# Optimization experiments

Measured on AMD Instinct MI355X. Metric: run time of the kernel, lower is better.

Reference implementation:

```python
import jax, jax.numpy as jnp
import numpy as np

L, N, E, D_MODEL, H = 3, 50000, 600000, 128, 8
D = D_MODEL // H          # per-head dim = 16
DFF = 4 * D_MODEL         # feedforward hidden = 512


def prelu(x, a):
    return jnp.where(x >= 0, x, a * x)


def layernorm(x, scale, bias, eps=1e-5):
    m = x.mean(-1, keepdims=True)
    v = x.var(-1, keepdims=True)
    return (x - m) * jax.lax.rsqrt(v + eps) * scale + bias


def setup_inputs() -> dict:
    key = jax.random.key(0)
    ks = jax.random.split(key, 16)
    s = 1.0 / np.sqrt(D_MODEL)
    return {
        "in_feats": jax.random.normal(ks[0], (N, D_MODEL), jnp.float32),
        "src": jax.random.randint(ks[1], (E,), 0, N, jnp.int32),
        "dst": jax.random.randint(ks[2], (E,), 0, N, jnp.int32),
        # per-layer stacked parameters
        "W": jax.random.normal(ks[3], (L, D_MODEL, D_MODEL), jnp.float32) * s,
        "attn_l": jax.random.normal(ks[4], (L, H, D), jnp.float32) * s,
        "attn_r": jax.random.normal(ks[5], (L, H, D), jnp.float32) * s,
        "conv_bias": jnp.zeros((L, H, D), jnp.float32),
        "a_conv": jnp.full((L,), 0.25, jnp.float32),   # PReLU slope after conv
        "ln_scale": jnp.ones((L, D_MODEL), jnp.float32),
        "ln_bias": jnp.zeros((L, D_MODEL), jnp.float32),
        "W1": jax.random.normal(ks[6], (L, D_MODEL, DFF), jnp.float32) * s,
        "b1": jnp.zeros((L, DFF), jnp.float32),
        "W2": jax.random.normal(ks[7], (L, DFF, D_MODEL), jnp.float32) / np.sqrt(DFF),
        "b2": jnp.zeros((L, D_MODEL), jnp.float32),
        "a_ff": jnp.full((L,), 0.25, jnp.float32),     # PReLU slope in FF
    }


def _gat_conv(x, src, dst, W, attn_l, attn_r, conv_bias, a_conv):
    # DGL GATConv: project, per-edge additive attention, edge-softmax over dst, scatter.
    z = (x @ W).reshape(N, H, D)                    # [N,H,D]
    el = (z * attn_l).sum(-1)                       # [N,H]
    er = (z * attn_r).sum(-1)                       # [N,H]
    e = jax.nn.leaky_relu(el[src] + er[dst], 0.2)   # [E,H]
    emax = jax.ops.segment_max(e, dst, num_segments=N)
    emax = jnp.where(jnp.isfinite(emax), emax, 0.0)  # zero in-degree guard
    ex = jnp.exp(e - emax[dst])                     # [E,H]
    denom = jax.ops.segment_sum(ex, dst, num_segments=N)  # [N,H]
    msg = ex[:, :, None] * z[src]                   # [E,H,D]
    agg = jax.ops.segment_sum(msg, dst, num_segments=N)   # [N,H,D]
    out = agg / jnp.maximum(denom, 1e-9)[:, :, None]
    out = prelu(out + conv_bias, a_conv)            # bias + PReLU activation
    return out.reshape(N, H * D)


def reference(in_feats, src, dst, W, attn_l, attn_r, conv_bias, a_conv,
              ln_scale, ln_bias, W1, b1, W2, b2, a_ff):
    outputs = []
    x = in_feats
    for l in range(L):
        h = _gat_conv(x, src, dst, W[l], attn_l[l], attn_r[l], conv_bias[l], a_conv[l])
        h = layernorm(h, ln_scale[l], ln_bias[l])   # layer['norm']
        # FeedForward, norm_first=True, sharing the same LayerNorm params
        hn = layernorm(h, ln_scale[l], ln_bias[l])
        ff = prelu(hn @ W1[l] + b1[l], a_ff[l]) @ W2[l] + b2[l]
        x = h + ff
        outputs.append(x)
    return jnp.stack(outputs)                       # [L, N, d]
```

## Files before the change

kernel.cpp:

```cpp
#include <hip/hip_runtime.h>

#define DM 128
#define NH 8
#define DFF 512

typedef __attribute__((ext_vector_type(8))) short bf16x8;
typedef __attribute__((ext_vector_type(4))) float f32x4;

#define WAITVM(N) do { asm volatile("s_waitcnt vmcnt(" #N ")" ::: "memory"); \
                       __builtin_amdgcn_sched_barrier(0); } while (0)

__device__ __forceinline__ short f2bf(float f) {
    union { float f; unsigned u; } v; v.f = f;
    unsigned r = v.u + 0x7fffu + ((v.u >> 16) & 1u);
    return (short)(r >> 16);
}
__device__ __forceinline__ float bf2f(unsigned short b) {
    union { unsigned u; float f; } v; v.u = ((unsigned)b) << 16; return v.f;
}

template<int ROWS, int NT>
__device__ __forceinline__ void stage_tile(
    const short* __restrict__ g, int row0, int maxrow, int rstride, int kbase,
    short* s, int tid)
{
    const int lane = tid & 63;
#pragma unroll
    for (int rr = 0; rr < ROWS * 16 / NT; ++rr) {
        int idx = rr * NT + tid;
        int row = idx >> 4, kc = idx & 15;
        int rg = row0 + row;
        rg = (rg < maxrow) ? rg : (maxrow - 1);
        const short* src = g + (size_t)rg * rstride + kbase
                         + ((kc ^ (row & 15)) << 3);
        short* dst = s + (size_t)(idx - lane) * 8;
        __builtin_amdgcn_global_load_lds(
            (const __attribute__((address_space(1))) void*)src,
            (__attribute__((address_space(3))) void*)dst, 16, 0, 0);
    }
}

__device__ __forceinline__ bf16x8 frag_ld(const short* s, int row, int ks, int g)
{
    return *(const bf16x8*)(s + row * 128 + ((((ks << 2) + g) ^ (row & 15)) << 3));
}

template<bool PRELU, int NOUT>
__global__ __launch_bounds__(512, 4) void gemm_k128_stream(
    const short* __restrict__ A, const short* __restrict__ Bt,
    const float* __restrict__ bias, const float* __restrict__ affp,
    int M, short* __restrict__ outbf)
{
    __shared__ __align__(16) short sW[128 * 128];
    __shared__ __align__(16) short sA[3][64 * 128];

    const int tid = threadIdx.x;
    const int wave = tid >> 6, lane = tid & 63;
    const int wm = wave >> 1, wn = wave & 1;
    const int bn = blockIdx.x * 128;
    const int fr = lane & 15, g = lane >> 4;
    const int lr4 = g << 2, lc = fr;
    const int nT = (M + 63) >> 6;
    const int GY = gridDim.y;
    const int t0 = blockIdx.y;
    const int nLoc = (t0 < nT) ? ((nT - 1 - t0) / GY + 1) : 0;

    float bb[4]; float aff = 0.0f;
    if constexpr (PRELU) {
        aff = *affp;
#pragma unroll
        for (int cg = 0; cg < 4; ++cg)
            bb[cg] = bias[bn + wn * 64 + cg * 16 + lc];
    }

    stage_tile<128, 512>(Bt + (size_t)bn * 128, 0, 128, 128, 0, sW, tid);
    if (nLoc > 0) stage_tile<64, 512>(A, t0 * 64, M, 128, 0, sA[0], tid);
    if (nLoc > 1) stage_tile<64, 512>(A, (t0 + GY) * 64, M, 128, 0, sA[1], tid);

    for (int i = 0; i < nLoc; ++i) {
        const int t = t0 + i * GY;
        if (i >= 1 && i + 1 < nLoc)
            stage_tile<64, 512>(A, (t + GY) * 64, M, 128, 0, sA[(i + 1) % 3], tid);

        if (i == 0) { if (nLoc > 1) WAITVM(2); else WAITVM(0); }
        else WAITVM(16);
        __builtin_amdgcn_s_barrier();

        const short* sAb = sA[i % 3];
        f32x4 acc[4];
#pragma unroll
        for (int cg = 0; cg < 4; ++cg) acc[cg] = (f32x4)0.0f;

#pragma unroll
        for (int ks = 0; ks < 4; ++ks) {
            bf16x8 af = frag_ld(sAb, wm * 16 + fr, ks, g);
#pragma unroll
            for (int cg = 0; cg < 4; ++cg) {
                bf16x8 bf = frag_ld(sW, wn * 64 + cg * 16 + fr, ks, g);
                acc[cg] = __builtin_amdgcn_mfma_f32_16x16x32_bf16(
                    af, bf, acc[cg], 0, 0, 0);
            }
        }

#pragma unroll
        for (int cg = 0; cg < 4; ++cg) {
            int colL = wn * 64 + cg * 16 + lc;
#pragma unroll
            for (int r = 0; r < 4; ++r) {
                int row = t * 64 + wm * 16 + lr4 + r;
                if (row < M) {
                    float v = acc[cg][r];
                    if constexpr (PRELU) {
                        v += bb[cg];
                        v = (v >= 0.0f) ? v : aff * v;
                    }
                    outbf[(size_t)row * NOUT + bn + colL] = f2bf(v);
                }
            }
        }
    }
}

__global__ __launch_bounds__(512) void ffn2_pipe(
    const short* __restrict__ H1, const short* __restrict__ W2t,
    const short* __restrict__ h_bf, const float* __restrict__ b2,
    int M, float* __restrict__ xo, short* __restrict__ xbf)
{
    __shared__ __align__(16) short sA[3][64 * 128];
    __shared__ __align__(16) short sB[3][128 * 128];

    const int tid = threadIdx.x;
    const int wave = tid >> 6, lane = tid & 63;
    const int wm = wave >> 1, wn = wave & 1;
    const int bm = blockIdx.x * 64;
    const int fr = lane & 15, g = lane >> 4;
    const int lr4 = g << 2, lc = fr;

    f32x4 acc[4];
#pragma unroll
    for (int cg = 0; cg < 4; ++cg) acc[cg] = (f32x4)0.0f;

    stage_tile<64, 512>(H1, bm, M, DFF, 0, sA[0], tid);
    stage_tile<128, 512>(W2t, 0, 128, DFF, 0, sB[0], tid);

#pragma unroll
    for (int c = 0; c < 4; ++c) {
        if (c < 3) {
            stage_tile<64, 512>(H1, bm, M, DFF, (c + 1) * 128, sA[(c + 1) % 3], tid);
            stage_tile<128, 512>(W2t, 0, 128, DFF, (c + 1) * 128, sB[(c + 1) % 3], tid);
        }
        if (c < 3) WAITVM(6); else WAITVM(0);
        __builtin_amdgcn_s_barrier();

        const short* a = sA[c % 3];
        const short* b = sB[c % 3];
#pragma unroll
        for (int ks = 0; ks < 4; ++ks) {
            bf16x8 af = frag_ld(a, wm * 16 + fr, ks, g);
#pragma unroll
            for (int cg = 0; cg < 4; ++cg) {
                bf16x8 bf = frag_ld(b, wn * 64 + cg * 16 + fr, ks, g);
                acc[cg] = __builtin_amdgcn_mfma_f32_16x16x32_bf16(
                    af, bf, acc[cg], 0, 0, 0);
            }
        }
    }

#pragma unroll
    for (int cg = 0; cg < 4; ++cg) {
        int colL = wn * 64 + cg * 16 + lc;
        float bbv = b2[colL];
#pragma unroll
        for (int r = 0; r < 4; ++r) {
            int row = bm + wm * 16 + lr4 + r;
            int rc = (row < M) ? row : (M - 1);
            float v = acc[cg][r] + bbv
                    + bf2f((unsigned short)h_bf[(size_t)rc * DM + colL]);
            if (row < M) {
                xo[(size_t)row * DM + colL]  = v;
                xbf[(size_t)row * DM + colL] = f2bf(v);
            }
        }
    }
}

__global__ void wt_conv_kernel(const float* __restrict__ in, short* __restrict__ out,
                               int R, int C, int nL)
{
    int idx = blockIdx.x * blockDim.x + threadIdx.x;
    if (idx >= nL * R * C) return;
    int l = idx / (R * C);
    int rem = idx - l * (R * C);
    int r = rem / C, c = rem - r * C;
    out[(size_t)l * R * C + (size_t)c * R + r] = f2bf(in[idx]);
}

__global__ void f2bf_kernel(const float* __restrict__ in, short* __restrict__ out, int n)
{
    int idx = blockIdx.x * blockDim.x + threadIdx.x;
    if (idx < n) out[idx] = f2bf(in[idx]);
}

__global__ void el_er_kernel(const short* __restrict__ z,
                             const float* __restrict__ al,
                             const float* __restrict__ ar,
                             float* __restrict__ el, float* __restrict__ er, int N)
{
    int idx = blockIdx.x * blockDim.x + threadIdx.x;
    if (idx >= N * NH) return;
    int n = idx >> 3, h = idx & 7;
    const unsigned* zp = (const unsigned*)(z + (size_t)n * DM + h * 16);
    const float* alp = al + h * 16;
    const float* arp = ar + h * 16;
    float sl = 0.0f, sr = 0.0f;
#pragma unroll
    for (int d2 = 0; d2 < 8; ++d2) {
        unsigned u = zp[d2];
        float z0 = bf2f((unsigned short)(u & 0xffff));
        float z1 = bf2f((unsigned short)(u >> 16));
        sl = fmaf(z0, alp[2 * d2], sl);     sl = fmaf(z1, alp[2 * d2 + 1], sl);
        sr = fmaf(z0, arp[2 * d2], sr);     sr = fmaf(z1, arp[2 * d2 + 1], sr);
    }
    el[idx] = sl;
    er[idx] = sr;
}

__global__ void hist_kernel(const int* __restrict__ dst, int* __restrict__ deg, int E)
{
    int e = blockIdx.x * blockDim.x + threadIdx.x;
    if (e < E) atomicAdd(&deg[dst[e]], 1);
}

__global__ void scan1_kernel(const int* __restrict__ deg, int* __restrict__ incl,
                             int* __restrict__ bsum, int N)
{
    __shared__ int sm[256];
    int i = blockIdx.x * 256 + threadIdx.x;
    int v = (i < N) ? deg[i] : 0;
    sm[threadIdx.x] = v;
    __syncthreads();
    for (int off = 1; off < 256; off <<= 1) {
        int t = (threadIdx.x >= off) ? sm[threadIdx.x - off] : 0;
        __syncthreads();
        sm[threadIdx.x] += t;
        __syncthreads();
    }
    if (i < N) incl[i] = sm[threadIdx.x];
    if (threadIdx.x == 255) bsum[blockIdx.x] = sm[255];
}

__global__ void scan2_kernel(int* __restrict__ bsum, int nb)
{
    __shared__ int sm[256];
    int v = (threadIdx.x < nb) ? bsum[threadIdx.x] : 0;
    sm[threadIdx.x] = v;
    __syncthreads();
    for (int off = 1; off < 256; off <<= 1) {
        int t = (threadIdx.x >= off) ? sm[threadIdx.x - off] : 0;
        __syncthreads();
        sm[threadIdx.x] += t;
        __syncthreads();
    }
    if (threadIdx.x < nb) bsum[threadIdx.x] = sm[threadIdx.x];
}

__global__ void scan3_kernel(const int* __restrict__ incl, const int* __restrict__ bsum,
                             int* __restrict__ row_ptr, int N)
{
    int i = blockIdx.x * 256 + threadIdx.x;
    if (i < N) {
        int off = (blockIdx.x > 0) ? bsum[blockIdx.x - 1] : 0;
        row_ptr[i + 1] = incl[i] + off;
    }
    if (i == 0) row_ptr[0] = 0;
}

__global__ void scatter_kernel(const int* __restrict__ src, const int* __restrict__ dst,
                               const int* __restrict__ row_ptr, int* __restrict__ cursor,
                               int* __restrict__ csr_src, int E)
{
    int e = blockIdx.x * blockDim.x + threadIdx.x;
    if (e >= E) return;
    int t = dst[e];
    int pos = atomicAdd(&cursor[t], 1);
    csr_src[row_ptr[t] + pos] = src[e];
}

__global__ __launch_bounds__(256) void gat_agg_ln_kernel(
    const int* __restrict__ row_ptr, const int* __restrict__ csr_src,
    const short* __restrict__ z, const float* __restrict__ el,
    const float* __restrict__ er, const float* __restrict__ cb,
    const float* __restrict__ a_conv,
    const float* __restrict__ scale, const float* __restrict__ bias,
    short* __restrict__ h_out, short* __restrict__ hn_out, int N)
{
    int wave = threadIdx.x >> 6, lane = threadIdx.x & 63;
    int t = blockIdx.x * 4 + wave;
    if (t >= N) return;
    int h = lane >> 3;
    int c0 = 2 * lane, c1 = c0 + 1;
    float er_t = er[t * NH + h];
    int e0 = row_ptr[t], e1 = row_ptr[t + 1];
    float acc0 = 0.0f, acc1 = 0.0f, den = 0.0f;
    const unsigned* zw = (const unsigned*)z;

    int e = e0;
    for (; e + 8 <= e1; e += 8) {
        int s[8];
#pragma unroll
        for (int k = 0; k < 8; ++k) s[k] = csr_src[e + k];
        float x[8]; unsigned u[8];
#pragma unroll
        for (int k = 0; k < 8; ++k) x[k] = el[s[k] * NH + h];
#pragma unroll
        for (int k = 0; k < 8; ++k) u[k] = zw[(size_t)s[k] * 64 + lane];
#pragma unroll
        for (int k = 0; k < 8; ++k) {
            float v = x[k] + er_t;
            v = (v >= 0.0f) ? v : 0.2f * v;
            float w = __expf(v);
            den += w;
            acc0 = fmaf(w, bf2f((unsigned short)(u[k] & 0xffff)), acc0);
            acc1 = fmaf(w, bf2f((unsigned short)(u[k] >> 16)),   acc1);
        }
    }
    for (; e + 4 <= e1; e += 4) {
        int s[4];
#pragma unroll
        for (int k = 0; k < 4; ++k) s[k] = csr_src[e + k];
        float x[4]; unsigned u[4];
#pragma unroll
        for (int k = 0; k < 4; ++k) x[k] = el[s[k] * NH + h];
#pragma unroll
        for (int k = 0; k < 4; ++k) u[k] = zw[(size_t)s[k] * 64 + lane];
#pragma unroll
        for (int k = 0; k < 4; ++k) {
            float v = x[k] + er_t;
            v = (v >= 0.0f) ? v : 0.2f * v;
            float w = __expf(v);
            den += w;
            acc0 = fmaf(w, bf2f((unsigned short)(u[k] & 0xffff)), acc0);
            acc1 = fmaf(w, bf2f((unsigned short)(u[k] >> 16)),   acc1);
        }
    }
    for (; e < e1; ++e) {
        int s = csr_src[e];
        float v = el[s * NH + h] + er_t;
        v = (v >= 0.0f) ? v : 0.2f * v;
        float w = __expf(v);
        den += w;
        unsigned u = zw[(size_t)s * 64 + lane];
        acc0 = fmaf(w, bf2f((unsigned short)(u & 0xffff)), acc0);
        acc1 = fmaf(w, bf2f((unsigned short)(u >> 16)), acc1);
    }

    float a = *a_conv;
    float inv = 1.0f / fmaxf(den, 1e-9f);
    float o0 = acc0 * inv + cb[c0];
    float o1 = acc1 * inv + cb[c1];
    o0 = (o0 >= 0.0f) ? o0 : a * o0;
    o1 = (o1 >= 0.0f) ? o1 : a * o1;

    float sc0 = scale[c0], sc1 = scale[c1];
    float bi0 = bias[c0], bi1 = bias[c1];

    float s1 = o0 + o1, ss = o0 * o0 + o1 * o1;
#pragma unroll
    for (int off = 32; off > 0; off >>= 1) {
        s1 += __shfl_xor(s1, off, 64);
        ss += __shfl_xor(ss, off, 64);
    }
    float mean = s1 * (1.0f / 128.0f);
    float var = ss * (1.0f / 128.0f) - mean * mean;
    float rstd = rsqrtf(var + 1e-5f);
    float h0 = (o0 - mean) * rstd * sc0 + bi0;
    float h1 = (o1 - mean) * rstd * sc1 + bi1;
    unsigned hlo = (unsigned short)f2bf(h0);
    unsigned hhi = (unsigned short)f2bf(h1);
    ((unsigned*)h_out)[(size_t)t * 64 + lane] = hlo | (hhi << 16);

    s1 = h0 + h1; ss = h0 * h0 + h1 * h1;
#pragma unroll
    for (int off = 32; off > 0; off >>= 1) {
        s1 += __shfl_xor(s1, off, 64);
        ss += __shfl_xor(ss, off, 64);
    }
    mean = s1 * (1.0f / 128.0f);
    var = ss * (1.0f / 128.0f) - mean * mean;
    rstd = rsqrtf(var + 1e-5f);
    unsigned lo = (unsigned short)f2bf((h0 - mean) * rstd * sc0 + bi0);
    unsigned hi = (unsigned short)f2bf((h1 - mean) * rstd * sc1 + bi1);
    ((unsigned*)hn_out)[(size_t)t * 64 + lane] = lo | (hi << 16);
}

extern "C" void kernel_launch(void* const* d_in, const int* in_sizes, int n_in,
                              void* d_out, int out_size, void* d_ws, size_t ws_size,
                              hipStream_t stream)
{
    const float* in_feats = (const float*)d_in[0];
    const int*   src      = (const int*)d_in[1];
    const int*   dst      = (const int*)d_in[2];
    const float* W        = (const float*)d_in[3];
    const float* attn_l   = (const float*)d_in[4];
    const float* attn_r   = (const float*)d_in[5];
    const float* convb    = (const float*)d_in[6];
    const float* a_conv   = (const float*)d_in[7];
    const float* ln_scale = (const float*)d_in[8];
    const float* ln_bias  = (const float*)d_in[9];
    const float* W1       = (const float*)d_in[10];
    const float* b1       = (const float*)d_in[11];
    const float* W2       = (const float*)d_in[12];
    const float* b2       = (const float*)d_in[13];
    const float* a_ff     = (const float*)d_in[14];
    float* out = (float*)d_out;

    const int N = in_sizes[0] / DM;
    const int E = in_sizes[1];
    const int L = in_sizes[7];

    char* wsb = (char*)d_ws;
    size_t off = 0;
    auto alloc = [&](size_t bytes) { char* p = wsb + off; off += (bytes + 255) & ~(size_t)255; return p; };

    short* z_bf  = (short*)alloc((size_t)N * DM * sizeof(short));
    short* h_bf  = (short*)alloc((size_t)N * DM * sizeof(short));
    short* hn_bf = (short*)alloc((size_t)N * DM * sizeof(short));
    short* x_bf  = (short*)alloc((size_t)N * DM * sizeof(short));
    short* H1    = (short*)alloc((size_t)N * DFF * sizeof(short));
    float* el    = (float*)alloc((size_t)N * NH * sizeof(float));
    float* er    = (float*)alloc((size_t)N * NH * sizeof(float));
    short* Wt    = (short*)alloc((size_t)L * DM * DM * sizeof(short));
    short* W1t   = (short*)alloc((size_t)L * DFF * DM * sizeof(short));
    short* W2t   = (short*)alloc((size_t)L * DM * DFF * sizeof(short));
    int* deg     = (int*)alloc((size_t)N * sizeof(int));
    int* incl    = (int*)alloc((size_t)N * sizeof(int));
    int* bsum    = (int*)alloc(256 * sizeof(int));
    int* row_ptr = (int*)alloc((size_t)(N + 1) * sizeof(int));
    int* cursor  = (int*)alloc((size_t)N * sizeof(int));
    int* csr_src = (int*)alloc((size_t)E * sizeof(int));

    const int gM64  = (N + 63) / 64;
    const int nbScan = (N + 255) / 256;

    hipMemsetAsync(deg, 0, (size_t)N * sizeof(int), stream);
    hipMemsetAsync(cursor, 0, (size_t)N * sizeof(int), stream);
    hist_kernel<<<(E + 255) / 256, 256, 0, stream>>>(dst, deg, E);
    scan1_kernel<<<nbScan, 256, 0, stream>>>(deg, incl, bsum, N);
    scan2_kernel<<<1, 256, 0, stream>>>(bsum, nbScan);
    scan3_kernel<<<nbScan, 256, 0, stream>>>(incl, bsum, row_ptr, N);
    scatter_kernel<<<(E + 255) / 256, 256, 0, stream>>>(src, dst, row_ptr, cursor, csr_src, E);

    wt_conv_kernel<<<(L * DM * DM + 255) / 256, 256, 0, stream>>>(W, Wt, DM, DM, L);
    wt_conv_kernel<<<(L * DM * DFF + 255) / 256, 256, 0, stream>>>(W1, W1t, DM, DFF, L);
    wt_conv_kernel<<<(L * DFF * DM + 255) / 256, 256, 0, stream>>>(W2, W2t, DFF, DM, L);
    f2bf_kernel<<<(N * DM + 255) / 256, 256, 0, stream>>>(in_feats, x_bf, N * DM);

    gemm_k128_stream<false, DM><<<dim3(1, 512), 512, 0, stream>>>(
        x_bf, Wt, nullptr, nullptr, N, z_bf);

    for (int l = 0; l < L; ++l) {
        float* xo = out + (size_t)l * N * DM;

        el_er_kernel<<<(N * NH + 255) / 256, 256, 0, stream>>>(
            z_bf, attn_l + (size_t)l * NH * 16, attn_r + (size_t)l * NH * 16, el, er, N);

        gat_agg_ln_kernel<<<(N + 3) / 4, 256, 0, stream>>>(
            row_ptr, csr_src, z_bf, el, er, convb + (size_t)l * DM, a_conv + l,
            ln_scale + (size_t)l * DM, ln_bias + (size_t)l * DM, h_bf, hn_bf, N);

        gemm_k128_stream<true, DFF><<<dim3(4, 128), 512, 0, stream>>>(
            hn_bf, W1t + (size_t)l * DFF * DM, b1 + (size_t)l * DFF, a_ff + l, N, H1);

        ffn2_pipe<<<gM64, 512, 0, stream>>>(
            H1, W2t + (size_t)l * DM * DFF, h_bf, b2 + (size_t)l * DM, N, xo, x_bf);

        if (l + 1 < L)
            gemm_k128_stream<false, DM><<<dim3(1, 512), 512, 0, stream>>>(
                x_bf, Wt + (size_t)(l + 1) * DM * DM, nullptr, nullptr, N, z_bf);
    }
}
```

Before: 506.3 us.

## Fuse next-layer projection into FFN2, retile GEMM waves, merge conversion kernels

```diff
diff --git a/kernel.cpp b/kernel.cpp
--- a/kernel.cpp
+++ b/kernel.cpp
@@ -8,6 +8,8 @@
 typedef __attribute__((ext_vector_type(4))) float f32x4;
 
 #define WAITVM(N) do { asm volatile("s_waitcnt vmcnt(" #N ")" ::: "memory"); \
+                       __builtin_amdgcn_sched_barrier(0); } while (0)
+#define WAITLGKM0 do { asm volatile("s_waitcnt lgkmcnt(0)" ::: "memory"); \
                        __builtin_amdgcn_sched_barrier(0); } while (0)
 
 __device__ __forceinline__ short f2bf(float f) {
@@ -56,21 +58,21 @@
 
     const int tid = threadIdx.x;
     const int wave = tid >> 6, lane = tid & 63;
-    const int wm = wave >> 1, wn = wave & 1;
+    const int wm = wave >> 2, wn = wave & 3;
     const int bn = blockIdx.x * 128;
     const int fr = lane & 15, g = lane >> 4;
-    const int lr4 = g << 2, lc = fr;
+    const int lr4 = g << 2;
     const int nT = (M + 63) >> 6;
     const int GY = gridDim.y;
     const int t0 = blockIdx.y;
     const int nLoc = (t0 < nT) ? ((nT - 1 - t0) / GY + 1) : 0;
 
-    float bb[4]; float aff = 0.0f;
+    float bb[2]; float aff = 0.0f;
     if constexpr (PRELU) {
         aff = *affp;
 #pragma unroll
-        for (int cg = 0; cg < 4; ++cg)
-            bb[cg] = bias[bn + wn * 64 + cg * 16 + lc];
+        for (int cg = 0; cg < 2; ++cg)
+            bb[cg] = bias[bn + wn * 32 + cg * 16 + fr];
     }
 
     stage_tile<128, 512>(Bt + (size_t)bn * 128, 0, 128, 128, 0, sW, tid);
@@ -82,123 +84,208 @@
         if (i >= 1 && i + 1 < nLoc)
             stage_tile<64, 512>(A, (t + GY) * 64, M, 128, 0, sA[(i + 1) % 3], tid);
 
-        if (i == 0) { if (nLoc > 1) WAITVM(2); else WAITVM(0); }
-        else WAITVM(16);
+        if (i == 0) { if (nLoc > 1) { WAITVM(2); } else { WAITVM(0); } }
+        else if (i + 1 < nLoc) { WAITVM(18); }
+        else { WAITVM(16); }
         __builtin_amdgcn_s_barrier();
 
         const short* sAb = sA[i % 3];
-        f32x4 acc[4];
-#pragma unroll
-        for (int cg = 0; cg < 4; ++cg) acc[cg] = (f32x4)0.0f;
+        f32x4 acc[2][2];
+#pragma unroll
+        for (int ii = 0; ii < 2; ++ii)
+#pragma unroll
+            for (int cg = 0; cg < 2; ++cg) acc[ii][cg] = (f32x4)0.0f;
 
 #pragma unroll
         for (int ks = 0; ks < 4; ++ks) {
-            bf16x8 af = frag_ld(sAb, wm * 16 + fr, ks, g);
-#pragma unroll
-            for (int cg = 0; cg < 4; ++cg) {
-                bf16x8 bf = frag_ld(sW, wn * 64 + cg * 16 + fr, ks, g);
-                acc[cg] = __builtin_amdgcn_mfma_f32_16x16x32_bf16(
-                    af, bf, acc[cg], 0, 0, 0);
-            }
-        }
-
-#pragma unroll
-        for (int cg = 0; cg < 4; ++cg) {
-            int colL = wn * 64 + cg * 16 + lc;
-#pragma unroll
-            for (int r = 0; r < 4; ++r) {
-                int row = t * 64 + wm * 16 + lr4 + r;
-                if (row < M) {
-                    float v = acc[cg][r];
-                    if constexpr (PRELU) {
-                        v += bb[cg];
-                        v = (v >= 0.0f) ? v : aff * v;
+            bf16x8 af[2], bf[2];
+#pragma unroll
+            for (int ii = 0; ii < 2; ++ii)
+                af[ii] = frag_ld(sAb, wm * 32 + ii * 16 + fr, ks, g);
+#pragma unroll
+            for (int cg = 0; cg < 2; ++cg)
+                bf[cg] = frag_ld(sW, wn * 32 + cg * 16 + fr, ks, g);
+#pragma unroll
+            for (int ii = 0; ii < 2; ++ii)
+#pragma unroll
+                for (int cg = 0; cg < 2; ++cg)
+                    acc[ii][cg] = __builtin_amdgcn_mfma_f32_16x16x32_bf16(
+                        af[ii], bf[cg], acc[ii][cg], 0, 0, 0);
+        }
+
+#pragma unroll
+        for (int ii = 0; ii < 2; ++ii)
+#pragma unroll
+            for (int cg = 0; cg < 2; ++cg) {
+                int colL = wn * 32 + cg * 16 + fr;
+#pragma unroll
+                for (int r = 0; r < 4; ++r) {
+                    int row = t * 64 + wm * 32 + ii * 16 + lr4 + r;
+                    if (row < M) {
+                        float v = acc[ii][cg][r];
+                        if constexpr (PRELU) {
+                            v += bb[cg];
+                            v = (v >= 0.0f) ? v : aff * v;
+                        }
+                        outbf[(size_t)row * NOUT + bn + colL] = f2bf(v);
                     }
-                    outbf[(size_t)row * NOUT + bn + colL] = f2bf(v);
                 }
             }
-        }
-    }
-}
-
-__global__ __launch_bounds__(512) void ffn2_pipe(
+    }
+}
+
+__global__ __launch_bounds__(512, 2) void ffn2z(
     const short* __restrict__ H1, const short* __restrict__ W2t,
     const short* __restrict__ h_bf, const float* __restrict__ b2,
-    int M, float* __restrict__ xo, short* __restrict__ xbf)
-{
-    __shared__ __align__(16) short sA[3][64 * 128];
-    __shared__ __align__(16) short sB[3][128 * 128];
+    const short* __restrict__ Wnt, int has_next, int M,
+    float* __restrict__ xo, short* __restrict__ z_next)
+{
+    __shared__ __align__(16) short sWn[128 * 128];
+    __shared__ __align__(16) short sA[2][64 * 128];
+    __shared__ __align__(16) short sB[2][128 * 128];
 
     const int tid = threadIdx.x;
     const int wave = tid >> 6, lane = tid & 63;
-    const int wm = wave >> 1, wn = wave & 1;
+    const int wm = wave >> 2, wn = wave & 3;
     const int bm = blockIdx.x * 64;
     const int fr = lane & 15, g = lane >> 4;
-    const int lr4 = g << 2, lc = fr;
-
-    f32x4 acc[4];
-#pragma unroll
-    for (int cg = 0; cg < 4; ++cg) acc[cg] = (f32x4)0.0f;
-
+    const int lr4 = g << 2;
+
+    f32x4 acc[2][2];
+#pragma unroll
+    for (int ii = 0; ii < 2; ++ii)
+#pragma unroll
+        for (int cg = 0; cg < 2; ++cg) acc[ii][cg] = (f32x4)0.0f;
+
+    stage_tile<128, 512>(Wnt, 0, 128, DM, 0, sWn, tid);
     stage_tile<64, 512>(H1, bm, M, DFF, 0, sA[0], tid);
     stage_tile<128, 512>(W2t, 0, 128, DFF, 0, sB[0], tid);
 
 #pragma unroll
     for (int c = 0; c < 4; ++c) {
+        __builtin_amdgcn_s_barrier();
         if (c < 3) {
-            stage_tile<64, 512>(H1, bm, M, DFF, (c + 1) * 128, sA[(c + 1) % 3], tid);
-            stage_tile<128, 512>(W2t, 0, 128, DFF, (c + 1) * 128, sB[(c + 1) % 3], tid);
-        }
-        if (c < 3) WAITVM(6); else WAITVM(0);
+            stage_tile<64, 512>(H1, bm, M, DFF, (c + 1) * 128, sA[(c + 1) & 1], tid);
+            stage_tile<128, 512>(W2t, 0, 128, DFF, (c + 1) * 128, sB[(c + 1) & 1], tid);
+            WAITVM(6);
+        } else {
+            WAITVM(0);
+        }
         __builtin_amdgcn_s_barrier();
 
-        const short* a = sA[c % 3];
-        const short* b = sB[c % 3];
+        const short* a = sA[c & 1];
+        const short* b = sB[c & 1];
 #pragma unroll
         for (int ks = 0; ks < 4; ++ks) {
-            bf16x8 af = frag_ld(a, wm * 16 + fr, ks, g);
-#pragma unroll
-            for (int cg = 0; cg < 4; ++cg) {
-                bf16x8 bf = frag_ld(b, wn * 64 + cg * 16 + fr, ks, g);
-                acc[cg] = __builtin_amdgcn_mfma_f32_16x16x32_bf16(
-                    af, bf, acc[cg], 0, 0, 0);
+            bf16x8 af[2], bf[2];
+#pragma unroll
+            for (int ii = 0; ii < 2; ++ii)
+                af[ii] = frag_ld(a, wm * 32 + ii * 16 + fr, ks, g);
+#pragma unroll
+            for (int cg = 0; cg < 2; ++cg)
+                bf[cg] = frag_ld(b, wn * 32 + cg * 16 + fr, ks, g);
+#pragma unroll
+            for (int ii = 0; ii < 2; ++ii)
+#pragma unroll
+                for (int cg = 0; cg < 2; ++cg)
+                    acc[ii][cg] = __builtin_amdgcn_mfma_f32_16x16x32_bf16(
+                        af[ii], bf[cg], acc[ii][cg], 0, 0, 0);
+        }
+    }
+
+    short* sX = sA[0];
+#pragma unroll
+    for (int ii = 0; ii < 2; ++ii)
+#pragma unroll
+        for (int cg = 0; cg < 2; ++cg) {
+            int colL = wn * 32 + cg * 16 + fr;
+            float bbv = b2[colL];
+#pragma unroll
+            for (int r = 0; r < 4; ++r) {
+                int rowL = wm * 32 + ii * 16 + lr4 + r;
+                int row = bm + rowL;
+                int rc = (row < M) ? row : (M - 1);
+                float v = acc[ii][cg][r] + bbv
+                        + bf2f((unsigned short)h_bf[(size_t)rc * DM + colL]);
+                if (row < M) xo[(size_t)row * DM + colL] = v;
+                if (has_next) {
+                    int kc = colL >> 3;
+                    sX[rowL * 128 + ((kc ^ (rowL & 15)) << 3) + (colL & 7)]
+                        = f2bf(v);
+                }
             }
         }
-    }
-
-#pragma unroll
-    for (int cg = 0; cg < 4; ++cg) {
-        int colL = wn * 64 + cg * 16 + lc;
-        float bbv = b2[colL];
-#pragma unroll
-        for (int r = 0; r < 4; ++r) {
-            int row = bm + wm * 16 + lr4 + r;
-            int rc = (row < M) ? row : (M - 1);
-            float v = acc[cg][r] + bbv
-                    + bf2f((unsigned short)h_bf[(size_t)rc * DM + colL]);
-            if (row < M) {
-                xo[(size_t)row * DM + colL]  = v;
-                xbf[(size_t)row * DM + colL] = f2bf(v);
+    if (!has_next) return;
+
+    WAITLGKM0;
+    __builtin_amdgcn_s_barrier();
+
+    f32x4 acc3[2][2];
+#pragma unroll
+    for (int ii = 0; ii < 2; ++ii)
+#pragma unroll
+        for (int cg = 0; cg < 2; ++cg) acc3[ii][cg] = (f32x4)0.0f;
+
+#pragma unroll
+    for (int ks = 0; ks < 4; ++ks) {
+        bf16x8 af[2], bf[2];
+#pragma unroll
+        for (int ii = 0; ii < 2; ++ii)
+            af[ii] = frag_ld(sX, wm * 32 + ii * 16 + fr, ks, g);
+#pragma unroll
+        for (int cg = 0; cg < 2; ++cg)
+            bf[cg] = frag_ld(sWn, wn * 32 + cg * 16 + fr, ks, g);
+#pragma unroll
+        for (int ii = 0; ii < 2; ++ii)
+#pragma unroll
+            for (int cg = 0; cg < 2; ++cg)
+                acc3[ii][cg] = __builtin_amdgcn_mfma_f32_16x16x32_bf16(
+                    af[ii], bf[cg], acc3[ii][cg], 0, 0, 0);
+    }
+#pragma unroll
+    for (int ii = 0; ii < 2; ++ii)
+#pragma unroll
+        for (int cg = 0; cg < 2; ++cg) {
+            int colL = wn * 32 + cg * 16 + fr;
+#pragma unroll
+            for (int r = 0; r < 4; ++r) {
+                int row = bm + wm * 32 + ii * 16 + lr4 + r;
+                if (row < M)
+                    z_next[(size_t)row * DM + colL] = f2bf(acc3[ii][cg][r]);
             }
         }
-    }
-}
-
-__global__ void wt_conv_kernel(const float* __restrict__ in, short* __restrict__ out,
-                               int R, int C, int nL)
+}
+
+__global__ void conv_all_kernel(
+    const float* __restrict__ W, const float* __restrict__ W1,
+    const float* __restrict__ W2, const float* __restrict__ xin,
+    short* __restrict__ Wt, short* __restrict__ W1t, short* __restrict__ W2t,
+    short* __restrict__ xbf, int nFeat, int nL)
 {
     int idx = blockIdx.x * blockDim.x + threadIdx.x;
-    if (idx >= nL * R * C) return;
-    int l = idx / (R * C);
-    int rem = idx - l * (R * C);
-    int r = rem / C, c = rem - r * C;
-    out[(size_t)l * R * C + (size_t)c * R + r] = f2bf(in[idx]);
-}
-
-__global__ void f2bf_kernel(const float* __restrict__ in, short* __restrict__ out, int n)
-{
-    int idx = blockIdx.x * blockDim.x + threadIdx.x;
-    if (idx < n) out[idx] = f2bf(in[idx]);
+    const int n0 = nL * DM * DM, n1 = nL * DM * DFF, n2 = nL * DFF * DM;
+    if (idx < n0) {
+        int l = idx / (DM * DM), rem = idx & (DM * DM - 1);
+        int r = rem >> 7, c = rem & 127;
+        Wt[(size_t)l * DM * DM + c * DM + r] = f2bf(W[idx]);
+        return;
+    }
+    idx -= n0;
+    if (idx < n1) {
+        int l = idx / (DM * DFF), rem = idx & (DM * DFF - 1);
+        int r = rem >> 9, c = rem & 511;
+        W1t[(size_t)l * DM * DFF + (size_t)c * DM + r] = f2bf(W1[idx]);
+        return;
+    }
+    idx -= n1;
+    if (idx < n2) {
+        int l = idx / (DFF * DM), rem = idx & (DFF * DM - 1);
+        int r = rem >> 7, c = rem & 127;
+        W2t[(size_t)l * DFF * DM + (size_t)c * DFF + r] = f2bf(W2[idx]);
+        return;
+    }
+    idx -= n2;
+    if (idx < nFeat) xbf[idx] = f2bf(xin[idx]);
 }
 
 __global__ void el_er_kernel(const short* __restrict__ z,
@@ -305,15 +392,23 @@
     const unsigned* zw = (const unsigned*)z;
 
     int e = e0;
-    for (; e + 8 <= e1; e += 8) {
-        int s[8];
+    int s[8];
+    bool have = (e + 8 <= e1);
+    if (have) {
 #pragma unroll
         for (int k = 0; k < 8; ++k) s[k] = csr_src[e + k];
+    }
+    while (have) {
         float x[8]; unsigned u[8];
 #pragma unroll
         for (int k = 0; k < 8; ++k) x[k] = el[s[k] * NH + h];
 #pragma unroll
         for (int k = 0; k < 8; ++k) u[k] = zw[(size_t)s[k] * 64 + lane];
+        int en = e + 8;
+        bool hv2 = (en + 8 <= e1);
+        int sn[8];
+#pragma unroll
+        for (int k = 0; k < 8; ++k) sn[k] = hv2 ? csr_src[en + k] : 0;
 #pragma unroll
         for (int k = 0; k < 8; ++k) {
             float v = x[k] + er_t;
@@ -323,16 +418,19 @@
             acc0 = fmaf(w, bf2f((unsigned short)(u[k] & 0xffff)), acc0);
             acc1 = fmaf(w, bf2f((unsigned short)(u[k] >> 16)),   acc1);
         }
+#pragma unroll
+        for (int k = 0; k < 8; ++k) s[k] = sn[k];
+        e = en; have = hv2;
     }
     for (; e + 4 <= e1; e += 4) {
-        int s[4];
-#pragma unroll
-        for (int k = 0; k < 4; ++k) s[k] = csr_src[e + k];
+        int s4[4];
+#pragma unroll
+        for (int k = 0; k < 4; ++k) s4[k] = csr_src[e + k];
         float x[4]; unsigned u[4];
 #pragma unroll
-        for (int k = 0; k < 4; ++k) x[k] = el[s[k] * NH + h];
-#pragma unroll
-        for (int k = 0; k < 4; ++k) u[k] = zw[(size_t)s[k] * 64 + lane];
+        for (int k = 0; k < 4; ++k) x[k] = el[s4[k] * NH + h];
+#pragma unroll
+        for (int k = 0; k < 4; ++k) u[k] = zw[(size_t)s4[k] * 64 + lane];
 #pragma unroll
         for (int k = 0; k < 4; ++k) {
             float v = x[k] + er_t;
@@ -344,12 +442,12 @@
         }
     }
     for (; e < e1; ++e) {
-        int s = csr_src[e];
-        float v = el[s * NH + h] + er_t;
+        int sv = csr_src[e];
+        float v = el[sv * NH + h] + er_t;
         v = (v >= 0.0f) ? v : 0.2f * v;
         float w = __expf(v);
         den += w;
-        unsigned u = zw[(size_t)s * 64 + lane];
+        unsigned u = zw[(size_t)sv * 64 + lane];
         acc0 = fmaf(w, bf2f((unsigned short)(u & 0xffff)), acc0);
         acc1 = fmaf(w, bf2f((unsigned short)(u >> 16)), acc1);
     }
@@ -450,19 +548,21 @@
     scan3_kernel<<<nbScan, 256, 0, stream>>>(incl, bsum, row_ptr, N);
     scatter_kernel<<<(E + 255) / 256, 256, 0, stream>>>(src, dst, row_ptr, cursor, csr_src, E);
 
-    wt_conv_kernel<<<(L * DM * DM + 255) / 256, 256, 0, stream>>>(W, Wt, DM, DM, L);
-    wt_conv_kernel<<<(L * DM * DFF + 255) / 256, 256, 0, stream>>>(W1, W1t, DM, DFF, L);
-    wt_conv_kernel<<<(L * DFF * DM + 255) / 256, 256, 0, stream>>>(W2, W2t, DFF, DM, L);
-    f2bf_kernel<<<(N * DM + 255) / 256, 256, 0, stream>>>(in_feats, x_bf, N * DM);
+    {
+        int total = L * DM * DM + L * DM * DFF + L * DFF * DM + N * DM;
+        conv_all_kernel<<<(total + 255) / 256, 256, 0, stream>>>(
+            W, W1, W2, in_feats, Wt, W1t, W2t, x_bf, N * DM, L);
+    }
 
     gemm_k128_stream<false, DM><<<dim3(1, 512), 512, 0, stream>>>(
         x_bf, Wt, nullptr, nullptr, N, z_bf);
+    el_er_kernel<<<(N * NH + 255) / 256, 256, 0, stream>>>(
+        z_bf, attn_l, attn_r, el, er, N);
 
     for (int l = 0; l < L; ++l) {
         float* xo = out + (size_t)l * N * DM;
-
-        el_er_kernel<<<(N * NH + 255) / 256, 256, 0, stream>>>(
-            z_bf, attn_l + (size_t)l * NH * 16, attn_r + (size_t)l * NH * 16, el, er, N);
+        const int has_next = (l + 1 < L) ? 1 : 0;
+        const short* Wnt = has_next ? (Wt + (size_t)(l + 1) * DM * DM) : Wt;
 
         gat_agg_ln_kernel<<<(N + 3) / 4, 256, 0, stream>>>(
             row_ptr, csr_src, z_bf, el, er, convb + (size_t)l * DM, a_conv + l,
@@ -471,11 +571,13 @@
         gemm_k128_stream<true, DFF><<<dim3(4, 128), 512, 0, stream>>>(
             hn_bf, W1t + (size_t)l * DFF * DM, b1 + (size_t)l * DFF, a_ff + l, N, H1);
 
-        ffn2_pipe<<<gM64, 512, 0, stream>>>(
-            H1, W2t + (size_t)l * DM * DFF, h_bf, b2 + (size_t)l * DM, N, xo, x_bf);
-
-        if (l + 1 < L)
-            gemm_k128_stream<false, DM><<<dim3(1, 512), 512, 0, stream>>>(
-                x_bf, Wt + (size_t)(l + 1) * DM * DM, nullptr, nullptr, N, z_bf);
-    }
-}
+        ffn2z<<<gM64, 512, 0, stream>>>(
+            H1, W2t + (size_t)l * DM * DFF, h_bf, b2 + (size_t)l * DM,
+            Wnt, has_next, N, xo, z_bf);
+
+        if (has_next)
+            el_er_kernel<<<(N * NH + 255) / 256, 256, 0, stream>>>(
+                z_bf, attn_l + (size_t)(l + 1) * NH * 16,
+                attn_r + (size_t)(l + 1) * NH * 16, el, er, N);
+    }
+}
```

Measured after the change: 504.0 us. No clear change (-0.5%).
